# Kernel optimization log

Hardware: AMD Instinct MI355X
Metric: run time of the kernel (lower is better)

## Reference

```python
import jax, jax.numpy as jnp
import numpy as np

D_MODEL = 1024
N_HEADS = 16
NUM_KV_HEADS = 4
D_K = D_MODEL // N_HEADS
ROPE_BASE = 10000.0


def apply_rotary_emb(x, base=ROPE_BASE):
    # x: [B, H, T, D], half-split rotation over positions 0..T-1
    B, H, T, D = x.shape
    inv_freq = 1.0 / (base ** (jnp.arange(0, D, 2, dtype=jnp.float32) / D))  # [D/2]
    ang = jnp.arange(T, dtype=jnp.float32)[:, None] * inv_freq[None, :]      # [T, D/2]
    cos = jnp.cos(ang)[None, None].astype(x.dtype)
    sin = jnp.sin(ang)[None, None].astype(x.dtype)
    x1, x2 = x[..., : D // 2], x[..., D // 2 :]
    return jnp.concatenate([x1 * cos - x2 * sin, x2 * cos + x1 * sin], axis=-1)


def setup_inputs() -> dict:
    key = jax.random.key(0)
    ks = jax.random.split(key, 6)
    B, Tq, Tkv = 4, 2048, 2048
    query = jax.random.normal(ks[0], (B, Tq, D_MODEL), dtype=jnp.float32)
    key_value = jax.random.normal(ks[1], (B, Tkv, D_MODEL), dtype=jnp.float32)
    query_mask = jnp.ones((B, Tq), dtype=jnp.bool_)
    kv_mask = jnp.ones((B, Tkv), dtype=jnp.bool_)
    s = 0.02
    w_q = jax.random.normal(ks[2], (D_MODEL, D_MODEL), dtype=jnp.float32) * s
    w_k = jax.random.normal(ks[3], (NUM_KV_HEADS * D_K, D_MODEL), dtype=jnp.float32) * s
    w_v = jax.random.normal(ks[4], (NUM_KV_HEADS * D_K, D_MODEL), dtype=jnp.float32) * s
    w_out = jax.random.normal(ks[5], (D_MODEL, D_MODEL), dtype=jnp.float32) * s
    return {"query": query, "key_value": key_value, "query_mask": query_mask,
            "kv_mask": kv_mask, "w_q": w_q, "w_k": w_k, "w_v": w_v, "w_out": w_out}


def reference(query, key_value, query_mask, kv_mask, w_q, w_k, w_v, w_out):
    B, Tq, _ = query.shape
    Tkv = key_value.shape[1]
    group = N_HEADS // NUM_KV_HEADS
    # projections (torch Linear: x @ W.T)
    Q = (query @ w_q.T).reshape(B, Tq, N_HEADS, D_K).transpose(0, 2, 1, 3)        # [B,H,Tq,D]
    K = (key_value @ w_k.T).reshape(B, Tkv, NUM_KV_HEADS, D_K).transpose(0, 2, 1, 3)
    V = (key_value @ w_v.T).reshape(B, Tkv, NUM_KV_HEADS, D_K).transpose(0, 2, 1, 3)
    # RoPE on Q and K
    Q = apply_rotary_emb(Q)
    K = apply_rotary_emb(K)
    # GQA: repeat kv heads
    K = jnp.repeat(K, group, axis=1)  # [B,H,Tkv,D]
    V = jnp.repeat(V, group, axis=1)
    # mask: [B,1,Tq,Tkv]
    attn_mask = (kv_mask[:, None, None, :] & query_mask[:, None, :, None])
    scale = 1.0 / jnp.sqrt(jnp.asarray(D_K, dtype=Q.dtype))
    scores = jnp.einsum("bhqd,bhkd->bhqk", Q, K) * scale
    scores = jnp.where(attn_mask, scores, jnp.asarray(-jnp.inf, dtype=scores.dtype))
    attn = jax.nn.softmax(scores, axis=-1)
    out = jnp.einsum("bhqk,bhkd->bhqd", attn, V)
    out = out.transpose(0, 2, 1, 3).reshape(B, Tq, D_MODEL)
    out = out @ w_out.T
    return out
```

## Files before the change

### kernel.cpp

```cpp
#include <hip/hip_runtime.h>
#include <hip/hip_bf16.h>
#include <hip/hip_fp16.h>

#define B_    4
#define TQ    2048
#define TKV   2048
#define DM    1024
#define NH    16
#define NKV   4
#define DK    64

typedef _Float16 f16x8 __attribute__((ext_vector_type(8)));
typedef _Float16 f16x4 __attribute__((ext_vector_type(4)));
typedef float    f32x4 __attribute__((ext_vector_type(4)));
typedef float    f32x16 __attribute__((ext_vector_type(16)));

__device__ __forceinline__ void store1(float* p, float v) { *p = v; }
__device__ __forceinline__ void store1(__half* p, float v) {
  union { __half h; unsigned short u; } c; c.h = __float2half(v);
  *(unsigned short*)p = c.u;
}

__device__ __forceinline__ f16x4 load4h(const float* p) {
  float4 v = *(const float4*)p;
  f16x4 r;
  r[0] = (_Float16)v.x; r[1] = (_Float16)v.y;
  r[2] = (_Float16)v.z; r[3] = (_Float16)v.w;
  return r;
}
__device__ __forceinline__ f16x4 load4h(const __half* p) {
  return *(const f16x4*)p;
}

__device__ __forceinline__ unsigned pack2h(float a, float b) {
  auto pk = __builtin_amdgcn_cvt_pkrtz(a, b);
  unsigned u;
  __builtin_memcpy(&u, &pk, 4);
  return u;
}

__global__ void zero_out_kernel(float* out, int n) {
  int i = blockIdx.x * blockDim.x + threadIdx.x;
  if (i < n) out[i] = 0.0f;
}

#define GAP 40
template <typename AT, typename CT>
__global__ __launch_bounds__(256) void gemm_bt_mfma(
    const AT* __restrict__ A,
    const float* __restrict__ W0, const float* __restrict__ W1,
    CT* __restrict__ C0, CT* __restrict__ C1, int M, int N, int K) {
  __shared__ _Float16 As[2 * 128 * GAP];
  __shared__ _Float16 Ws[2 * 128 * GAP];
  const float* __restrict__ W = (blockIdx.z == 0) ? W0 : W1;
  CT* __restrict__ C = (blockIdx.z == 0) ? C0 : C1;

  const int t = threadIdx.x;
  const int w = t >> 6, l = t & 63;
  const int lm = l & 15, quad = l >> 4;
  const int wm = (w >> 1) * 64, wn = (w & 1) * 64;
  const int m0 = blockIdx.y * 128, n0 = blockIdx.x * 128;

  const int srow = t >> 3;
  const int scol = (t & 7) * 4;

  f32x4 acc[4][4] = {};
  f16x4 av[4], wv[4];
#pragma unroll
  for (int p = 0; p < 4; ++p) {
    int r = srow + p * 32;
    av[p] = load4h(&A[(size_t)(m0 + r) * K + scol]);
    wv[p] = load4h(&W[(size_t)(n0 + r) * K + scol]);
  }

  int cur = 0;
  for (int k0 = 0; k0 < K; k0 += 32) {
    _Float16* as = &As[cur * 128 * GAP];
    _Float16* ws = &Ws[cur * 128 * GAP];
#pragma unroll
    for (int p = 0; p < 4; ++p) {
      int r = srow + p * 32;
      *(f16x4*)&as[r * GAP + scol] = av[p];
      *(f16x4*)&ws[r * GAP + scol] = wv[p];
    }
    __syncthreads();
    if (k0 + 32 < K) {
#pragma unroll
      for (int p = 0; p < 4; ++p) {
        int r = srow + p * 32;
        av[p] = load4h(&A[(size_t)(m0 + r) * K + k0 + 32 + scol]);
        wv[p] = load4h(&W[(size_t)(n0 + r) * K + k0 + 32 + scol]);
      }
    }

    f16x8 af[4], bf[4];
#pragma unroll
    for (int i = 0; i < 4; ++i)
      af[i] = *(const f16x8*)&as[(wm + i * 16 + lm) * GAP + quad * 8];
#pragma unroll
    for (int j = 0; j < 4; ++j)
      bf[j] = *(const f16x8*)&ws[(wn + j * 16 + lm) * GAP + quad * 8];
#pragma unroll
    for (int i = 0; i < 4; ++i)
#pragma unroll
      for (int j = 0; j < 4; ++j)
        acc[i][j] =
            __builtin_amdgcn_mfma_f32_16x16x32_f16(af[i], bf[j], acc[i][j], 0, 0, 0);
    cur ^= 1;
  }

#pragma unroll
  for (int i = 0; i < 4; ++i)
#pragma unroll
    for (int r = 0; r < 4; ++r) {
      size_t row = (size_t)(m0 + wm + i * 16 + quad * 4 + r) * N;
#pragma unroll
      for (int j = 0; j < 4; ++j)
        store1(&C[row + n0 + wn + j * 16 + lm], acc[i][j][r]);
    }
}

__global__ void rope_kernel(__half* __restrict__ X, int T, int H, int total_pairs) {
  int idx = blockIdx.x * blockDim.x + threadIdx.x;
  if (idx >= total_pairs) return;
  int i   = idx & 31;
  int h   = (idx >> 5) % H;
  int row = idx / (32 * H);
  int tpos = row % T;
  __half* p = X + ((size_t)row * H + h) * DK;
  float inv = exp2f((float)i * -0.41524101186091403f);
  float ang = (float)tpos * inv;
  float c, s;
  sincosf(ang, &s, &c);
  float x1 = __half2float(p[i]), x2 = __half2float(p[i + 32]);
  p[i]      = __float2half(x1 * c - x2 * s);
  p[i + 32] = __float2half(x2 * c + x1 * s);
}

#define AP 72
#define C2 0.18033688011112042f
__global__ __launch_bounds__(256, 2) void attn_mfma(const __half* Q,
                                                    const __half* __restrict__ K,
                                                    const __half* __restrict__ V,
                                                    __half* O) {
  __shared__ _Float16 Ks[64 * AP];
  __shared__ _Float16 Vt[64 * AP];
  const int t = threadIdx.x;
  const int w = t >> 6, l = t & 63;
  const int lq = l & 31, hi = l >> 5;
  const int qt = blockIdx.x, h = blockIdx.y, b = blockIdx.z;
  const int kvh = h >> 2;

  const __half* qbase =
      Q + (((size_t)b * TQ + qt * 128 + w * 32 + lq) * NH + h) * DK;
  f16x8 aq[4];
#pragma unroll
  for (int kc = 0; kc < 4; ++kc)
    aq[kc] = *(const f16x8*)(qbase + kc * 16 + hi * 8);

  {
    const float tpos = (float)(qt * 128 + w * 32 + lq);
#pragma unroll
    for (int kc = 0; kc < 2; ++kc)
#pragma unroll
      for (int j = 0; j < 8; ++j) {
        int d = kc * 16 + hi * 8 + j;
        float inv = exp2f((float)d * -0.41524101186091403f);
        float ang = tpos * inv;
        float c, s;
        sincosf(ang, &s, &c);
        float x1 = (float)aq[kc][j], x2 = (float)aq[kc + 2][j];
        aq[kc][j]     = (_Float16)(x1 * c - x2 * s);
        aq[kc + 2][j] = (_Float16)(x2 * c + x1 * s);
      }
  }

  const f16x8 vones = {1.f16, 1.f16, 1.f16, 1.f16, 1.f16, 1.f16, 1.f16, 1.f16};

  const int skey = t >> 3, sdseg = t & 7;
  const int vkey = t & 63, vdb0 = (t >> 6) * 8;
  const __half* kp0 =
      K + (((size_t)b * TKV + skey) * NKV + kvh) * DK + sdseg * 8;
  const __half* kp1 = kp0 + (size_t)32 * NKV * DK;
  const __half* vp0 =
      V + (((size_t)b * TKV + vkey) * NKV + kvh) * DK + vdb0;
  const __half* vp1 = vp0 + 32;
  const size_t kstep = (size_t)64 * NKV * DK;

  f16x8 kpre0 = *(const f16x8*)kp0, kpre1 = *(const f16x8*)kp1;
  f16x8 vpre0 = *(const f16x8*)vp0, vpre1 = *(const f16x8*)vp1;

  f32x16 o_acc[2], l_acc;
#pragma unroll
  for (int i = 0; i < 16; ++i) { o_acc[0][i] = 0.f; o_acc[1][i] = 0.f; l_acc[i] = 0.f; }
  float m_run = -1e30f;

  for (int ck = 0; ck < TKV / 64; ++ck) {
    __syncthreads();
    *(f16x8*)&Ks[skey * AP + sdseg * 8] = kpre0;
    *(f16x8*)&Ks[(skey + 32) * AP + sdseg * 8] = kpre1;
#pragma unroll
    for (int j = 0; j < 8; ++j) {
      Vt[(vdb0 + j) * AP + vkey] = vpre0[j];
      Vt[(vdb0 + 32 + j) * AP + vkey] = vpre1[j];
    }
    __syncthreads();
    if (ck + 1 < TKV / 64) {
      size_t off = (size_t)(ck + 1) * kstep;
      kpre0 = *(const f16x8*)(kp0 + off);
      kpre1 = *(const f16x8*)(kp1 + off);
      vpre0 = *(const f16x8*)(vp0 + off);
      vpre1 = *(const f16x8*)(vp1 + off);
    }

    f32x16 st[2];
#pragma unroll
    for (int i = 0; i < 16; ++i) { st[0][i] = 0.f; st[1][i] = 0.f; }
    __builtin_amdgcn_s_setprio(1);
#pragma unroll
    for (int tile = 0; tile < 2; ++tile)
#pragma unroll
      for (int kc = 0; kc < 4; ++kc) {
        f16x8 ak =
            *(const f16x8*)&Ks[(tile * 32 + lq) * AP + kc * 16 + hi * 8];
        st[tile] =
            __builtin_amdgcn_mfma_f32_32x32x16_f16(ak, aq[kc], st[tile], 0, 0, 0);
      }
    __builtin_amdgcn_s_setprio(0);

    float vmax = st[0][0];
#pragma unroll
    for (int i = 1; i < 16; ++i) vmax = fmaxf(vmax, st[0][i]);
#pragma unroll
    for (int i = 0; i < 16; ++i) vmax = fmaxf(vmax, st[1][i]);
    vmax *= C2;
    vmax = fmaxf(vmax, __shfl_xor(vmax, 32));

    if (!__all(vmax - m_run <= 8.0f)) {
      float m_new = fmaxf(m_run, vmax);
      float alpha = exp2f(m_run - m_new);
      m_run = m_new;
#pragma unroll
      for (int reg = 0; reg < 16; ++reg) {
        int row = (reg & 3) + 8 * (reg >> 2) + 4 * hi;
        float ar = __shfl(alpha, row);
        l_acc[reg] *= ar;
        o_acc[0][reg] *= ar;
        o_acc[1][reg] *= ar;
      }
    }

    unsigned q16u[2][8];
#pragma unroll
    for (int tile = 0; tile < 2; ++tile)
#pragma unroll
      for (int rr = 0; rr < 8; ++rr) {
        float p0 = exp2f(st[tile][2 * rr] * C2 - m_run);
        float p1 = exp2f(st[tile][2 * rr + 1] * C2 - m_run);
        q16u[tile][rr] = pack2h(p0, p1);
      }

    __builtin_amdgcn_s_setprio(1);
#pragma unroll
    for (int kb = 0; kb < 4; ++kb) {
      const int tl = kb >> 1, base = (kb & 1) * 4;
      union { unsigned u[4]; f16x8 v; } ap;
#pragma unroll
      for (int c = 0; c < 2; ++c) {
        unsigned R0 = q16u[tl][base + c];
        unsigned R1 = q16u[tl][base + 2 + c];
        unsigned Z = hi ? R0 : R1;
        unsigned Xp = __shfl_xor(Z, 32);
        ap.u[c]     = hi ? Xp : R0;
        ap.u[c + 2] = hi ? R1 : Xp;
      }
      l_acc = __builtin_amdgcn_mfma_f32_32x32x16_f16(ap.v, vones, l_acc, 0, 0, 0);
#pragma unroll
      for (int nt = 0; nt < 2; ++nt) {
        f16x8 bv = *(const f16x8*)&Vt[(nt * 32 + lq) * AP + kb * 16 + hi * 8];
        o_acc[nt] =
            __builtin_amdgcn_mfma_f32_32x32x16_f16(ap.v, bv, o_acc[nt], 0, 0, 0);
      }
    }
    __builtin_amdgcn_s_setprio(0);
  }

#pragma unroll
  for (int reg = 0; reg < 16; ++reg) {
    int row = (reg & 3) + 8 * (reg >> 2) + 4 * hi;
    float inv = 1.0f / l_acc[reg];
    size_t orow =
        (((size_t)b * TQ + qt * 128 + w * 32 + row) * NH + h) * DK;
    O[orow + lq]      = __float2half(o_acc[0][reg] * inv);
    O[orow + 32 + lq] = __float2half(o_acc[1][reg] * inv);
  }
}

extern "C" void kernel_launch(void* const* d_in, const int* in_sizes, int n_in,
                              void* d_out, int out_size, void* d_ws, size_t ws_size,
                              hipStream_t stream) {
  int iq, ikv, iwq, iwk, iwv, iwo;
  bool ok = true;
  if (n_in >= 8 && in_sizes[0] == 8388608 && in_sizes[1] == 8388608) {
    iq = 0; ikv = 1; iwq = 4; iwk = 5; iwv = 6; iwo = 7;
  } else if (n_in >= 8 && in_sizes[0] == 8388608 && in_sizes[1] == 8192) {
    ikv = 0; iq = 2; iwk = 4; iwo = 5; iwq = 6; iwv = 7;
  } else if (n_in == 6 && in_sizes[2] == 1048576) {
    iq = 0; ikv = 1; iwq = 2; iwk = 3; iwv = 4; iwo = 5;
  } else if (n_in == 6 && in_sizes[2] == 262144) {
    ikv = 0; iq = 1; iwk = 2; iwo = 3; iwq = 4; iwv = 5;
  } else {
    ok = false; iq = ikv = iwq = iwk = iwv = iwo = 0;
  }

  const size_t nQ  = (size_t)B_ * TQ * DM;
  const size_t nKV = (size_t)B_ * TKV * NKV * DK;
  const size_t need = (nQ + 2 * nKV) * sizeof(__half);
  if (!ok || ws_size < need) {
    zero_out_kernel<<<(out_size + 255) / 256, 256, 0, stream>>>((float*)d_out,
                                                                out_size);
    return;
  }

  const float* query     = (const float*)d_in[iq];
  const float* key_value = (const float*)d_in[ikv];
  const float* w_q   = (const float*)d_in[iwq];
  const float* w_k   = (const float*)d_in[iwk];
  const float* w_v   = (const float*)d_in[iwv];
  const float* w_out = (const float*)d_in[iwo];
  float* out = (float*)d_out;

  __half* Qh = (__half*)d_ws;
  __half* Kh = Qh + nQ;
  __half* Vh = Kh + nKV;

  dim3 blk(256);
  gemm_bt_mfma<<<dim3(DM / 128, B_ * TQ / 128, 1), blk, 0, stream>>>(
      query, w_q, w_q, Qh, Qh, B_ * TQ, DM, DM);
  gemm_bt_mfma<<<dim3(NKV * DK / 128, B_ * TKV / 128, 2), blk, 0, stream>>>(
      key_value, w_k, w_v, Kh, Vh, B_ * TKV, NKV * DK, DM);
  int pk = B_ * TKV * NKV * 32;
  rope_kernel<<<(pk + 255) / 256, blk, 0, stream>>>(Kh, TKV, NKV, pk);
  attn_mfma<<<dim3(TQ / 128, NH, B_), dim3(256), 0, stream>>>(Qh, Kh, Vh, Qh);
  gemm_bt_mfma<<<dim3(DM / 128, B_ * TQ / 128, 1), blk, 0, stream>>>(
      Qh, w_out, w_out, out, out, B_ * TQ, DM, DM);
}
```

Measured before the change: 382.7 us.

## Fuse K RoPE into projection GEMM epilogue, prescale Q, widen half loads

Drops the standalone RoPE kernel for K and applies the rotation in the K/V projection GEMM epilogue while values are still in fp32 accumulators. The softmax scale is folded into Q during its in-kernel RoPE, which removes one multiply per score in the attention loop. The GEMM now loads half-precision A operands with 8-wide vector loads and converts fp32 through packed cvt instructions. Attention launch bounds are raised to 4 blocks per CU, which may force register spilling.

```diff
diff --git a/kernel.cpp b/kernel.cpp
--- a/kernel.cpp
+++ b/kernel.cpp
@@ -15,21 +15,13 @@
 typedef float    f32x4 __attribute__((ext_vector_type(4)));
 typedef float    f32x16 __attribute__((ext_vector_type(16)));
 
+template <typename T> struct IsHalf { static constexpr bool v = false; };
+template <> struct IsHalf<__half> { static constexpr bool v = true; };
+
 __device__ __forceinline__ void store1(float* p, float v) { *p = v; }
 __device__ __forceinline__ void store1(__half* p, float v) {
   union { __half h; unsigned short u; } c; c.h = __float2half(v);
   *(unsigned short*)p = c.u;
-}
-
-__device__ __forceinline__ f16x4 load4h(const float* p) {
-  float4 v = *(const float4*)p;
-  f16x4 r;
-  r[0] = (_Float16)v.x; r[1] = (_Float16)v.y;
-  r[2] = (_Float16)v.z; r[3] = (_Float16)v.w;
-  return r;
-}
-__device__ __forceinline__ f16x4 load4h(const __half* p) {
-  return *(const f16x4*)p;
 }
 
 __device__ __forceinline__ unsigned pack2h(float a, float b) {
@@ -39,17 +31,26 @@
   return u;
 }
 
+__device__ __forceinline__ f16x4 load4h(const float* p) {
+  float4 v = *(const float4*)p;
+  union { unsigned u[2]; f16x4 h; } c;
+  c.u[0] = pack2h(v.x, v.y);
+  c.u[1] = pack2h(v.z, v.w);
+  return c.h;
+}
+
 __global__ void zero_out_kernel(float* out, int n) {
   int i = blockIdx.x * blockDim.x + threadIdx.x;
   if (i < n) out[i] = 0.0f;
 }
 
 #define GAP 40
+#define RLOG2 -0.41524101186091403f
 template <typename AT, typename CT>
 __global__ __launch_bounds__(256) void gemm_bt_mfma(
     const AT* __restrict__ A,
     const float* __restrict__ W0, const float* __restrict__ W1,
-    CT* __restrict__ C0, CT* __restrict__ C1, int M, int N, int K) {
+    CT* __restrict__ C0, CT* __restrict__ C1, int M, int N, int K, int ropeT) {
   __shared__ _Float16 As[2 * 128 * GAP];
   __shared__ _Float16 Ws[2 * 128 * GAP];
   const float* __restrict__ W = (blockIdx.z == 0) ? W0 : W1;
@@ -61,37 +62,56 @@
   const int wm = (w >> 1) * 64, wn = (w & 1) * 64;
   const int m0 = blockIdx.y * 128, n0 = blockIdx.x * 128;
 
-  const int srow = t >> 3;
-  const int scol = (t & 7) * 4;
+  const int srow = t >> 3, scol = (t & 7) * 4;
+  const int hrow = t >> 2, hcol = (t & 3) * 8;
 
   f32x4 acc[4][4] = {};
-  f16x4 av[4], wv[4];
-#pragma unroll
-  for (int p = 0; p < 4; ++p) {
-    int r = srow + p * 32;
-    av[p] = load4h(&A[(size_t)(m0 + r) * K + scol]);
-    wv[p] = load4h(&W[(size_t)(n0 + r) * K + scol]);
-  }
-
+  f16x4 av4[4], wv4[4];
+  f16x8 av8[2];
+
+  auto loadA = [&](int k0) {
+    if constexpr (IsHalf<AT>::v) {
+#pragma unroll
+      for (int p = 0; p < 2; ++p)
+        av8[p] = *(const f16x8*)&A[(size_t)(m0 + hrow + p * 64) * K + k0 + hcol];
+    } else {
+#pragma unroll
+      for (int p = 0; p < 4; ++p)
+        av4[p] = load4h(&A[(size_t)(m0 + srow + p * 32) * K + k0 + scol]);
+    }
+  };
+  auto storeA = [&](_Float16* as) {
+    if constexpr (IsHalf<AT>::v) {
+#pragma unroll
+      for (int p = 0; p < 2; ++p)
+        *(f16x8*)&as[(hrow + p * 64) * GAP + hcol] = av8[p];
+    } else {
+#pragma unroll
+      for (int p = 0; p < 4; ++p)
+        *(f16x4*)&as[(srow + p * 32) * GAP + scol] = av4[p];
+    }
+  };
+  auto loadW = [&](int k0) {
+#pragma unroll
+    for (int p = 0; p < 4; ++p)
+      wv4[p] = load4h(&W[(size_t)(n0 + srow + p * 32) * K + k0 + scol]);
+  };
+  auto storeW = [&](_Float16* ws) {
+#pragma unroll
+    for (int p = 0; p < 4; ++p)
+      *(f16x4*)&ws[(srow + p * 32) * GAP + scol] = wv4[p];
+  };
+
+  loadA(0);
+  loadW(0);
   int cur = 0;
   for (int k0 = 0; k0 < K; k0 += 32) {
     _Float16* as = &As[cur * 128 * GAP];
     _Float16* ws = &Ws[cur * 128 * GAP];
-#pragma unroll
-    for (int p = 0; p < 4; ++p) {
-      int r = srow + p * 32;
-      *(f16x4*)&as[r * GAP + scol] = av[p];
-      *(f16x4*)&ws[r * GAP + scol] = wv[p];
-    }
+    storeA(as);
+    storeW(ws);
     __syncthreads();
-    if (k0 + 32 < K) {
-#pragma unroll
-      for (int p = 0; p < 4; ++p) {
-        int r = srow + p * 32;
-        av[p] = load4h(&A[(size_t)(m0 + r) * K + k0 + 32 + scol]);
-        wv[p] = load4h(&W[(size_t)(n0 + r) * K + k0 + 32 + scol]);
-      }
-    }
+    if (k0 + 32 < K) { loadA(k0 + 32); loadW(k0 + 32); }
 
     f16x8 af[4], bf[4];
 #pragma unroll
@@ -109,6 +129,27 @@
     cur ^= 1;
   }
 
+  if (ropeT != 0 && blockIdx.z == 0) {
+    float inv0 = exp2f((float)lm * RLOG2);
+    float inv1 = exp2f((float)(16 + lm) * RLOG2);
+#pragma unroll
+    for (int i = 0; i < 4; ++i)
+#pragma unroll
+      for (int r = 0; r < 4; ++r) {
+        int row = m0 + wm + i * 16 + quad * 4 + r;
+        float tpos = (float)(row & (ropeT - 1));
+        float c0, s0, c1, s1;
+        sincosf(tpos * inv0, &s0, &c0);
+        sincosf(tpos * inv1, &s1, &c1);
+        float x0 = acc[i][0][r], y0 = acc[i][2][r];
+        acc[i][0][r] = x0 * c0 - y0 * s0;
+        acc[i][2][r] = y0 * c0 + x0 * s0;
+        float x1 = acc[i][1][r], y1 = acc[i][3][r];
+        acc[i][1][r] = x1 * c1 - y1 * s1;
+        acc[i][3][r] = y1 * c1 + x1 * s1;
+      }
+  }
+
 #pragma unroll
   for (int i = 0; i < 4; ++i)
 #pragma unroll
@@ -120,26 +161,9 @@
     }
 }
 
-__global__ void rope_kernel(__half* __restrict__ X, int T, int H, int total_pairs) {
-  int idx = blockIdx.x * blockDim.x + threadIdx.x;
-  if (idx >= total_pairs) return;
-  int i   = idx & 31;
-  int h   = (idx >> 5) % H;
-  int row = idx / (32 * H);
-  int tpos = row % T;
-  __half* p = X + ((size_t)row * H + h) * DK;
-  float inv = exp2f((float)i * -0.41524101186091403f);
-  float ang = (float)tpos * inv;
-  float c, s;
-  sincosf(ang, &s, &c);
-  float x1 = __half2float(p[i]), x2 = __half2float(p[i + 32]);
-  p[i]      = __float2half(x1 * c - x2 * s);
-  p[i + 32] = __float2half(x2 * c + x1 * s);
-}
-
 #define AP 72
 #define C2 0.18033688011112042f
-__global__ __launch_bounds__(256, 2) void attn_mfma(const __half* Q,
+__global__ __launch_bounds__(256, 4) void attn_mfma(const __half* Q,
                                                     const __half* __restrict__ K,
                                                     const __half* __restrict__ V,
                                                     __half* O) {
@@ -165,13 +189,13 @@
 #pragma unroll
       for (int j = 0; j < 8; ++j) {
         int d = kc * 16 + hi * 8 + j;
-        float inv = exp2f((float)d * -0.41524101186091403f);
+        float inv = exp2f((float)d * RLOG2);
         float ang = tpos * inv;
         float c, s;
         sincosf(ang, &s, &c);
         float x1 = (float)aq[kc][j], x2 = (float)aq[kc + 2][j];
-        aq[kc][j]     = (_Float16)(x1 * c - x2 * s);
-        aq[kc + 2][j] = (_Float16)(x2 * c + x1 * s);
+        aq[kc][j]     = (_Float16)((x1 * c - x2 * s) * C2);
+        aq[kc + 2][j] = (_Float16)((x2 * c + x1 * s) * C2);
       }
   }
 
@@ -233,7 +257,6 @@
     for (int i = 1; i < 16; ++i) vmax = fmaxf(vmax, st[0][i]);
 #pragma unroll
     for (int i = 0; i < 16; ++i) vmax = fmaxf(vmax, st[1][i]);
-    vmax *= C2;
     vmax = fmaxf(vmax, __shfl_xor(vmax, 32));
 
     if (!__all(vmax - m_run <= 8.0f)) {
@@ -255,8 +278,8 @@
     for (int tile = 0; tile < 2; ++tile)
 #pragma unroll
       for (int rr = 0; rr < 8; ++rr) {
-        float p0 = exp2f(st[tile][2 * rr] * C2 - m_run);
-        float p1 = exp2f(st[tile][2 * rr + 1] * C2 - m_run);
+        float p0 = exp2f(st[tile][2 * rr] - m_run);
+        float p1 = exp2f(st[tile][2 * rr + 1] - m_run);
         q16u[tile][rr] = pack2h(p0, p1);
       }
 
@@ -336,12 +359,10 @@
 
   dim3 blk(256);
   gemm_bt_mfma<<<dim3(DM / 128, B_ * TQ / 128, 1), blk, 0, stream>>>(
-      query, w_q, w_q, Qh, Qh, B_ * TQ, DM, DM);
+      query, w_q, w_q, Qh, Qh, B_ * TQ, DM, DM, 0);
   gemm_bt_mfma<<<dim3(NKV * DK / 128, B_ * TKV / 128, 2), blk, 0, stream>>>(
-      key_value, w_k, w_v, Kh, Vh, B_ * TKV, NKV * DK, DM);
-  int pk = B_ * TKV * NKV * 32;
-  rope_kernel<<<(pk + 255) / 256, blk, 0, stream>>>(Kh, TKV, NKV, pk);
+      key_value, w_k, w_v, Kh, Vh, B_ * TKV, NKV * DK, DM, TKV);
   attn_mfma<<<dim3(TQ / 128, NH, B_), dim3(256), 0, stream>>>(Qh, Kh, Vh, Qh);
   gemm_bt_mfma<<<dim3(DM / 128, B_ * TQ / 128, 1), blk, 0, stream>>>(
-      Qh, w_out, w_out, out, out, B_ * TQ, DM, DM);
-}
+      Qh, w_out, w_out, out, out, B_ * TQ, DM, DM, 0);
+}
```

After: 465.2 us. 21.6% more time.
